# Kernel optimization log

Measured on AMD Instinct MI355X. Metric: run time of the kernel, lower is better.

Reference implementation:

```python
import jax, jax.numpy as jnp
import numpy as np

KSIZE = 3
SCALE = 10.0
EPS = 1e-4


def _prelu(x, a):
    return jnp.where(x >= 0, x, a * x)


def _conv1x1(x, w, b):
    # x: [B,C,H,W], w: [O,C], b: [O]
    return jnp.einsum('bchw,oc->bohw', x, w) + b[None, :, None, None]


def _extract_patches(x, k):
    # same-padded kxk patches, torch-unfold channel-major ordering.
    # x: [B,C,H,W] -> [B, H*W, C, k, k]
    B, C, H, W = x.shape
    p = k // 2
    xp = jnp.pad(x, ((0, 0), (0, 0), (p, p), (p, p)))
    pats = jnp.stack([xp[:, :, i:i + H, j:j + W]
                      for i in range(k) for j in range(k)], axis=2)  # [B,C,k*k,H,W]
    pats = pats.reshape(B, C, k, k, H * W)
    return jnp.transpose(pats, (0, 4, 1, 2, 3))


def setup_inputs() -> dict:
    key = jax.random.key(0)
    ks = jax.random.split(key, 10)
    B, C, r = 4, 64, 2
    H = W = 96
    h = w = 48
    Cr = C // r
    s = 0.05
    return {
        'input': jax.random.normal(ks[0], (B, C, H, W), jnp.float32),
        'small': jax.random.normal(ks[1], (B, C, h, w), jnp.float32),
        'w_match1': jax.random.normal(ks[2], (Cr, C), jnp.float32) * s,
        'b_match1': jax.random.normal(ks[3], (Cr,), jnp.float32) * s,
        'a_match1': jnp.full((1,), 0.25, jnp.float32),
        'w_match2': jax.random.normal(ks[4], (Cr, C), jnp.float32) * s,
        'b_match2': jax.random.normal(ks[5], (Cr,), jnp.float32) * s,
        'a_match2': jnp.full((1,), 0.25, jnp.float32),
        'w_asm': jax.random.normal(ks[6], (C, C), jnp.float32) * s,
        'b_asm': jax.random.normal(ks[7], (C,), jnp.float32) * s,
        'a_asm': jnp.full((1,), 0.25, jnp.float32),
    }


def reference(input, small, w_match1, b_match1, a_match1,
              w_match2, b_match2, a_match2, w_asm, b_asm, a_asm):
    dn = ('NCHW', 'OIHW', 'NCHW')
    pad1 = [(1, 1), (1, 1)]

    match_input = _prelu(_conv1x1(input, w_match1, b_match1), a_match1)  # [B,Cr,H,W]
    embed_w = _prelu(_conv1x1(small, w_asm, b_asm), a_asm)               # [B,C,h,w]
    ref = _prelu(_conv1x1(small, w_match2, b_match2), a_match2)          # [B,Cr,h,w]

    raw_w = _extract_patches(embed_w, KSIZE)  # [B, L, C, 3, 3]  (reconstruction filters)
    w_pat = _extract_patches(ref, KSIZE)      # [B, L, Cr, 3, 3] (matching filters)

    def per_sample(xi, wi, raw_wi):
        # xi: [Cr,H,W], wi: [L,Cr,3,3], raw_wi: [L,C,3,3]
        norm = jnp.sqrt(jnp.sum(wi * wi, axis=(1, 2, 3), keepdims=True))
        wi_n = wi / jnp.maximum(norm, EPS)
        # dynamic conv: correlation of xi with all L normalized patches
        yi = jax.lax.conv_general_dilated(xi[None], wi_n, (1, 1), pad1,
                                          dimension_numbers=dn)  # [1,L,H,W]
        yi = jax.nn.softmax(yi * SCALE, axis=1)
        # conv_transpose2d(yi, raw_wi, stride=2, padding=1):
        # lhs_dilation=2, pad k-1-p=1, spatially flipped, in/out swapped kernel
        wt = jnp.transpose(raw_wi, (1, 0, 2, 3))[:, :, ::-1, ::-1]  # [C,L,3,3]
        out = jax.lax.conv_general_dilated(yi, wt, (1, 1), pad1,
                                           lhs_dilation=(2, 2),
                                           dimension_numbers=dn)  # [1,C,2H-1,2W-1]
        return out[0] / 6.0

    return jax.vmap(per_sample)(match_input, w_pat, raw_w)
```

## Files before the change

kernel.cpp:

```cpp
#include <hip/hip_runtime.h>


typedef unsigned short u16;
typedef __attribute__((ext_vector_type(8))) short short8;
typedef __attribute__((ext_vector_type(8))) _Float16 half8;
typedef __attribute__((ext_vector_type(4))) float f32x4;

__device__ __forceinline__ u16 f2bf(float f) {
    unsigned u = __float_as_uint(f);
    unsigned r = (u + 0x7FFFu + ((u >> 16) & 1u)) >> 16;
    return (u16)r;
}
__device__ __forceinline__ float bf2f(u16 h) {
    return __uint_as_float(((unsigned)h) << 16);
}
__device__ __forceinline__ u16 f2h(float f) {
    _Float16 h = (_Float16)f;
    u16 u; __builtin_memcpy(&u, &h, 2); return u;
}
__device__ __forceinline__ float h2f(u16 u) {
    _Float16 h; __builtin_memcpy(&h, &u, 2); return (float)h;
}

__global__ void kzero(float4* p, long n) {
    long i = (long)blockIdx.x * blockDim.x + threadIdx.x;
    long st = (long)gridDim.x * blockDim.x;
    float4 z; z.x = 0.f; z.y = 0.f; z.z = 0.f; z.w = 0.f;
    for (; i < n; i += st) p[i] = z;
}

__global__ void kmatch(const float* __restrict__ input, const float* __restrict__ w1,
                       const float* __restrict__ b1, const float* __restrict__ a1,
                       u16* __restrict__ xf16) {
    __shared__ float xl[64 * 96];
    __shared__ float wl[32 * 65];
    int b = blockIdx.x / 96, y = blockIdx.x % 96;
    int tid = threadIdx.x;
    for (int i = tid; i < 64 * 96; i += 256) {
        int ci = i / 96, xx = i % 96;
        xl[i] = input[(((b * 64 + ci) * 96) + y) * 96 + xx];
    }
    for (int i = tid; i < 2048; i += 256) wl[(i >> 6) * 65 + (i & 63)] = w1[i];
    __syncthreads();
    float aa = a1[0];
    for (int o = tid; o < 96 * 32; o += 256) {
        int xx = o >> 5, c = o & 31;
        float acc = b1[c];
        #pragma unroll
        for (int ci = 0; ci < 64; ci++) acc = fmaf(xl[ci * 96 + xx], wl[c * 65 + ci], acc);
        float v = acc >= 0.f ? acc : aa * acc;
        xf16[((b * 98 + y + 1) * 98 + (xx + 1)) * 32 + c] = f2h(v);
    }
}

__global__ void ksmall(const float* __restrict__ small, const float* __restrict__ wasm,
                       const float* __restrict__ basm, const float* __restrict__ aasm,
                       const float* __restrict__ wm2, const float* __restrict__ bm2,
                       const float* __restrict__ am2,
                       float* __restrict__ ef32, u16* __restrict__ rkl) {
    __shared__ float sl[64 * 48];
    __shared__ float wa[64 * 65];
    __shared__ float wm[32 * 65];
    int b = blockIdx.x / 48, y = blockIdx.x % 48;
    int tid = threadIdx.x;
    for (int i = tid; i < 64 * 48; i += 256) {
        int ci = i / 48, xx = i % 48;
        sl[i] = small[(((b * 64 + ci) * 48) + y) * 48 + xx];
    }
    for (int i = tid; i < 4096; i += 256) wa[(i >> 6) * 65 + (i & 63)] = wasm[i];
    for (int i = tid; i < 2048; i += 256) wm[(i >> 6) * 65 + (i & 63)] = wm2[i];
    __syncthreads();
    float ae = aasm[0], ar = am2[0];
    for (int o = tid; o < 48 * 64; o += 256) {
        int xx = o >> 6, c = o & 63;
        float acc = basm[c];
        #pragma unroll
        for (int ci = 0; ci < 64; ci++) acc = fmaf(sl[ci * 48 + xx], wa[c * 65 + ci], acc);
        float v = acc >= 0.f ? acc : ae * acc;
        ef32[((b * 50 + y + 1) * 50 + (xx + 1)) * 64 + c] = v;
    }
    for (int o = tid; o < 48 * 32; o += 256) {
        int xx = o >> 5, c = o & 31;
        float acc = bm2[c];
        #pragma unroll
        for (int ci = 0; ci < 64; ci++) acc = fmaf(sl[ci * 48 + xx], wm[c * 65 + ci], acc);
        float v = acc >= 0.f ? acc : ar * acc;
        rkl[((b * 50 + y + 1) * 50 + (xx + 1)) * 32 + c] = f2h(v);
    }
}

__global__ void kinvnorm(const u16* __restrict__ rkl, float* __restrict__ invn) {
    int idx = blockIdx.x * 256 + threadIdx.x;
    int b = idx / 2304, l = idx % 2304;
    int ly = l / 48, lx = l % 48;
    float s = 0.f;
    for (int ty = 0; ty < 3; ty++)
        for (int tx = 0; tx < 3; tx++) {
            int base = ((b * 50 + ly + ty) * 50 + (lx + tx)) * 32;
            #pragma unroll
            for (int c = 0; c < 32; c++) {
                float v = h2f(rkl[base + c]);
                s = fmaf(v, v, s);
            }
        }
    invn[idx] = 10.f / fmaxf(sqrtf(s), 1e-4f);
}

__global__ void kvtp(const float* __restrict__ ef32, u16* __restrict__ vtp) {
    __shared__ float el[3][50 * 64];
    int bi = blockIdx.x;
    int b = bi / 48, ly = bi % 48;
    const float* eb = ef32 + (size_t)b * 50 * 50 * 64;
    int tid = threadIdx.x;
    #pragma unroll
    for (int r = 0; r < 3; ++r)
        for (int i = tid; i < 800; i += 256)
            ((float4*)el[r])[i] = ((const float4*)(eb + (size_t)(ly + r) * 3200))[i];
    __syncthreads();
    u16* vo = vtp + (size_t)b * 576 * 2304 + (size_t)ly * 48;
    for (int n = tid; n < 576; n += 256) {
        int t = n >> 6, c = n & 63;
        int ty = t / 3, tx = t - ty * 3;
        u16* dst = vo + (size_t)n * 2304;
        const float* src = &el[ty][tx * 64 + c];
        #pragma unroll
        for (int g = 0; g < 12; ++g) {
            unsigned lo = (unsigned)f2bf(src[(g * 4 + 0) * 64]) |
                          ((unsigned)f2bf(src[(g * 4 + 1) * 64]) << 16);
            unsigned hi = (unsigned)f2bf(src[(g * 4 + 2) * 64]) |
                          ((unsigned)f2bf(src[(g * 4 + 3) * 64]) << 16);
            uint2 pk; pk.x = lo; pk.y = hi;
            *(uint2*)&dst[g * 4] = pk;
        }
    }
}

__device__ __forceinline__ void stage_ks4(const u16* __restrict__ src, u16* dst, int tid) {
    int wb = tid & ~63;
    #pragma unroll
    for (int k = 0; k < 3; ++k)
        __builtin_amdgcn_global_load_lds(
            (const __attribute__((address_space(1))) void*)(src + (size_t)(tid + k * 256) * 8),
            (__attribute__((address_space(3))) void*)(dst + (size_t)(wb + k * 256) * 8),
            16, 0, 0);
    if (tid < 32)
        __builtin_amdgcn_global_load_lds(
            (const __attribute__((address_space(1))) void*)(src + (size_t)(tid + 768) * 8),
            (__attribute__((address_space(3))) void*)(dst + (size_t)768 * 8),
            16, 0, 0);
}
__device__ __forceinline__ void stage_ks2(const u16* __restrict__ src, u16* dst, int tid) {
    int wb = tid & ~63;
    __builtin_amdgcn_global_load_lds(
        (const __attribute__((address_space(1))) void*)(src + (size_t)tid * 8),
        (__attribute__((address_space(3))) void*)(dst + (size_t)wb * 8),
        16, 0, 0);
    if (tid < 144)
        __builtin_amdgcn_global_load_lds(
            (const __attribute__((address_space(1))) void*)(src + (size_t)(tid + 256) * 8),
            (__attribute__((address_space(3))) void*)(dst + (size_t)(wb + 256) * 8),
            16, 0, 0);
}

__launch_bounds__(256, 2)
__global__ void kfused3(const u16* __restrict__ xf16, const u16* __restrict__ rkl,
                        const u16* __restrict__ vtp, const float* __restrict__ invn,
                        float* __restrict__ Z, int b0, int nb) {
    __shared__ u16 Ks[6][1600];
    __shared__ u16 Pl[2][4608];
    __shared__ u16 Qs[5 * 18 * 32];
    __shared__ float llds[4][16];

    int tid = threadIdx.x;
    int w = tid >> 6, lane = tid & 63, l15 = lane & 15, quad = lane >> 4;
    int bi = blockIdx.x, brel, t;
    if (nb == 4) { brel = bi & 3; t = bi >> 2; }
    else         { brel = 0; t = bi; }
    int b = b0 + brel;
    int px0 = (t % 6) * 16, pyb = (t / 6) * 3;

    const u16* xb = xf16 + (size_t)b * 98 * 98 * 32;
    const u16* rb = rkl + (size_t)b * 50 * 50 * 32;
    const float* invb = invn + b * 2304;
    const u16* vw = vtp + (size_t)b * 576 * 2304 + (size_t)(w * 144 + l15) * 2304 + quad * 8;

    stage_ks4(rb, &Ks[0][0], tid);
    __builtin_amdgcn_sched_barrier(0);

    for (int u = tid; u < 360; u += 256) {
        int cell = u >> 2, ch = u & 3;
        int r = cell / 18, p = cell % 18;
        *(short8*)&Qs[(r * 18 + p) * 32 + ch * 8] =
            *(const short8*)(xb + (((pyb + r) * 98) + (px0 + p)) * 32 + ch * 8);
    }

    int tile = (w < 3) ? w : 2;
    int kh_begin = (w == 3) ? 1 : 0;
    int kh_end   = (w == 2) ? 1 : 2;

    f32x4 acc[27];
    #pragma unroll
    for (int i = 0; i < 27; i++) acc[i] = (f32x4)0.f;
    float lacc[4] = {0.f, 0.f, 0.f, 0.f};

    __syncthreads();

    short8 vv[9];
    int s0 = 0;

    for (int it = 0; it < 24; ++it) {
        int ly0 = it * 2;
        int cur = it & 1;

        float pinv[2][3];
        #pragma unroll
        for (int kh = 0; kh < 2; ++kh)
            #pragma unroll
            for (int lxo = 0; lxo < 3; ++lxo)
                pinv[kh][lxo] = invb[(ly0 + kh) * 48 + lxo * 16 + l15];

        if (it < 23) {
            int s4 = s0 + 4; if (s4 >= 6) s4 -= 6;
            stage_ks2(rb + (size_t)(ly0 + 4) * 1600, &Ks[0][0] + s4 * 1600, tid);
        }
        __builtin_amdgcn_sched_barrier(0x38F);

        const u16* vit = vw + it * 96;
        #pragma unroll
        for (int nt = 0; nt < 9; ++nt) vv[nt] = *(const short8*)(vit + (size_t)nt * 36864);

        u16* Pc = Pl[cur];
        #pragma unroll
        for (int kh = 0; kh < 2; ++kh) {
            if (kh < kh_begin || kh >= kh_end) continue;
            f32x4 sf[3];
            #pragma unroll
            for (int i = 0; i < 3; i++) sf[i] = (f32x4)0.f;
            __builtin_amdgcn_s_setprio(1);
            #pragma unroll
            for (int ty = 0; ty < 3; ++ty) {
                int rr = s0 + kh + ty; if (rr >= 6) rr -= 6;
                const u16* Kr = &Ks[0][0] + rr * 1600;
                #pragma unroll
                for (int tx = 0; tx < 3; ++tx) {
                    half8 a = *(const half8*)&Qs[((tile + ty) * 18 + (l15 + tx)) * 32 + quad * 8];
                    #pragma unroll
                    for (int lxo = 0; lxo < 3; ++lxo) {
                        half8 bb = *(const half8*)&Kr[(lxo * 16 + l15 + tx) * 32 + quad * 8];
                        sf[lxo] = __builtin_amdgcn_mfma_f32_16x16x32_f16(a, bb, sf[lxo], 0, 0, 0);
                    }
                }
            }
            __builtin_amdgcn_s_setprio(0);
            #pragma unroll
            for (int lxo = 0; lxo < 3; ++lxo) {
                float invs = pinv[kh][lxo];
                int k = kh * 48 + lxo * 16 + l15;
                int kb = k >> 5;
                int kc = (k & 31) ^ (quad << 3);
                #pragma unroll
                for (int r = 0; r < 4; ++r) {
                    float p = __expf(sf[lxo][r] * invs);
                    u16 h = f2bf(p);
                    Pc[(tile * 3 + kb) * 512 + (quad * 4 + r) * 32 + kc] = h;
                    lacc[r] += bf2f(h);
                }
            }
        }

        asm volatile("s_waitcnt vmcnt(9) lgkmcnt(0)" ::: "memory");
        __builtin_amdgcn_s_barrier();
        __builtin_amdgcn_sched_barrier(0);

        const u16* Pr = Pl[cur];
        int pcol = l15 * 32 + ((quad ^ (l15 >> 2)) & 3) * 8;
        __builtin_amdgcn_s_setprio(1);
        #pragma unroll
        for (int ks = 0; ks < 3; ++ks) {
            short8 pa0 = *(const short8*)&Pr[(0 * 3 + ks) * 512 + pcol];
            short8 pa1 = *(const short8*)&Pr[(1 * 3 + ks) * 512 + pcol];
            short8 pa2 = *(const short8*)&Pr[(2 * 3 + ks) * 512 + pcol];
            #pragma unroll
            for (int nt = 0; nt < 9; ++nt) {
                short8 vn = vv[nt];
                acc[0 * 9 + nt] = __builtin_amdgcn_mfma_f32_16x16x32_bf16(pa0, vn, acc[0 * 9 + nt], 0, 0, 0);
                acc[1 * 9 + nt] = __builtin_amdgcn_mfma_f32_16x16x32_bf16(pa1, vn, acc[1 * 9 + nt], 0, 0, 0);
                acc[2 * 9 + nt] = __builtin_amdgcn_mfma_f32_16x16x32_bf16(pa2, vn, acc[2 * 9 + nt], 0, 0, 0);
                if (ks < 2)
                    vv[nt] = *(const short8*)(vit + (size_t)nt * 36864 + (ks + 1) * 32);
            }
        }
        __builtin_amdgcn_s_setprio(0);

        s0 += 2; if (s0 >= 6) s0 -= 6;
    }

    #pragma unroll
    for (int r = 0; r < 4; ++r) {
        float v = lacc[r];
        v += __shfl_xor(v, 1);
        v += __shfl_xor(v, 2);
        v += __shfl_xor(v, 4);
        v += __shfl_xor(v, 8);
        lacc[r] = v;
    }
    if (l15 == 0) {
        #pragma unroll
        for (int r = 0; r < 4; ++r)
            llds[w][quad * 4 + r] = lacc[r];
    }
    __syncthreads();
    float* Zb = Z + (size_t)brel * 9216 * 576;
    #pragma unroll
    for (int mt = 0; mt < 3; ++mt) {
        #pragma unroll
        for (int r = 0; r < 4; ++r) {
            int q = (pyb + mt) * 96 + px0 + quad * 4 + r;
            float lsum = (mt < 2) ? llds[mt][quad * 4 + r]
                                  : (llds[2][quad * 4 + r] + llds[3][quad * 4 + r]);
            float rl = 1.0f / (lsum * 6.0f);
            float* zr = Zb + (size_t)q * 576 + w * 144;
            #pragma unroll
            for (int nt = 0; nt < 9; ++nt)
                __builtin_nontemporal_store(acc[mt * 9 + nt][r] * rl, zr + nt * 16 + l15);
        }
    }
}

__global__ void kgather(const float* __restrict__ Z, float* __restrict__ out, int b0) {
    __shared__ float zb[2 * 9 * 580];
    int bi = blockIdx.x;
    int brel = bi / (96 * 12);
    int rem = bi % (96 * 12);
    int b = b0 + brel;
    int q = rem / 12, xt = rem % 12;
    int ox0 = xt * 16, p0 = ox0 >> 1;
    const float* Zb = Z + (size_t)brel * 9216 * 576;
    int tid = threadIdx.x;
    for (int id = tid; id < 2592; id += 256) {
        int pi = id / 1296, r2 = id % 1296;
        int pxi = r2 / 144, n4 = r2 % 144;
        int py = q + pi; if (py > 95) py = 95;
        int px = p0 + pxi; if (px > 95) px = 95;
        *(float4*)&zb[(pi * 9 + pxi) * 580 + n4 * 4] =
            *(const float4*)&Zb[(size_t)(py * 96 + px) * 576 + n4 * 4];
    }
    __syncthreads();
    int xi = tid & 15, cq = tid >> 4;
    int ox = ox0 + xi;
    bool oxv = ox <= 190;
    int ntx, txl[2], pxl[2];
    if (xi & 1) { ntx = 2; txl[0] = 0; pxl[0] = (xi + 1) >> 1; txl[1] = 2; pxl[1] = (xi - 1) >> 1; }
    else        { ntx = 1; txl[0] = 1; pxl[0] = xi >> 1; txl[1] = 1; pxl[1] = xi >> 1; }
    int oy0 = 2 * q;
    #pragma unroll
    for (int ck = 0; ck < 4; ++ck) {
        int c = cq + ck * 16;
        float v0 = 0.f, v1 = 0.f;
        for (int j = 0; j < ntx; ++j) {
            int tx = txl[j], pxi = pxl[j];
            v0 += zb[(0 * 9 + pxi) * 580 + (3 + tx) * 64 + c];
            v1 += zb[(1 * 9 + pxi) * 580 + (0 + tx) * 64 + c];
            v1 += zb[(0 * 9 + pxi) * 580 + (6 + tx) * 64 + c];
        }
        if (oxv) {
            float* o = out + (((size_t)(b * 64 + c) * 191 + oy0) * 191 + ox);
            *o = v0;
            if (q < 95) *(o + 191) = v1;
        }
    }
}

extern "C" void kernel_launch(void* const* d_in, const int* in_sizes, int n_in,
                              void* d_out, int out_size, void* d_ws, size_t ws_size,
                              hipStream_t stream) {
    const float* input = (const float*)d_in[0];
    const float* small = (const float*)d_in[1];
    const float* w1 = (const float*)d_in[2];
    const float* b1 = (const float*)d_in[3];
    const float* a1 = (const float*)d_in[4];
    const float* w2 = (const float*)d_in[5];
    const float* b2 = (const float*)d_in[6];
    const float* a2 = (const float*)d_in[7];
    const float* wa = (const float*)d_in[8];
    const float* ba = (const float*)d_in[9];
    const float* aa = (const float*)d_in[10];

    char* ws = (char*)d_ws;
    u16* xf16 = (u16*)(ws + 0);
    u16* rkl = (u16*)(ws + 2458624);
    float* ef = (float*)(ws + 3098624);
    u16* vtp = (u16*)(ws + 5658624);
    float* invn = (float*)(ws + 16275456);
    const size_t PREP = 16312320;
    float* Zbuf = (float*)(ws + PREP);
    float* out = (float*)d_out;

    int nb = (ws_size >= (size_t)101246976) ? 4 : 1;

    kzero<<<1024, 256, 0, stream>>>((float4*)ws, 5658624 / 16);
    kmatch<<<384, 256, 0, stream>>>(input, w1, b1, a1, xf16);
    ksmall<<<192, 256, 0, stream>>>(small, wa, ba, aa, w2, b2, a2, ef, rkl);
    kinvnorm<<<36, 256, 0, stream>>>(rkl, invn);
    kvtp<<<192, 256, 0, stream>>>(ef, vtp);

    for (int b0 = 0; b0 < 4; b0 += nb) {
        kfused3<<<nb * 192, 256, 0, stream>>>(xf16, rkl, vtp, invn, Zbuf, b0, nb);
        kgather<<<nb * 1152, 256, 0, stream>>>(Zbuf, out, b0);
    }
}
```

Baseline: 471.1 us.

## Process four key rows per iteration with one key row per wave

The main loop now handles four key rows per iteration, 12 iterations instead of 24. Each wave owns one key row and computes scores for all three query tiles, so the uneven tile/kh split across waves is gone. The K ring buffer grows to 10 rows and the P buffer doubles so each PV step covers a 192-wide K chunk. Softmax partial sums are now kept per tile and summed across all four waves. Per-iteration barriers are halved, at the cost of much more LDS per block, which could limit occupancy, and more register pressure.

```diff
diff --git a/kernel.cpp b/kernel.cpp
--- a/kernel.cpp
+++ b/kernel.cpp
@@ -166,10 +166,10 @@
 __global__ void kfused3(const u16* __restrict__ xf16, const u16* __restrict__ rkl,
                         const u16* __restrict__ vtp, const float* __restrict__ invn,
                         float* __restrict__ Z, int b0, int nb) {
-    __shared__ u16 Ks[6][1600];
-    __shared__ u16 Pl[2][4608];
+    __shared__ u16 Ks[10][1600];
+    __shared__ u16 Pl[2][9216];
     __shared__ u16 Qs[5 * 18 * 32];
-    __shared__ float llds[4][16];
+    __shared__ float llds[4][3][16];
 
     int tid = threadIdx.x;
     int w = tid >> 6, lane = tid & 63, l15 = lane & 15, quad = lane >> 4;
@@ -185,6 +185,7 @@
     const u16* vw = vtp + (size_t)b * 576 * 2304 + (size_t)(w * 144 + l15) * 2304 + quad * 8;
 
     stage_ks4(rb, &Ks[0][0], tid);
+    stage_ks2(rb + (size_t)4 * 1600, &Ks[4][0], tid);
     __builtin_amdgcn_sched_barrier(0);
 
     for (int u = tid; u < 360; u += 256) {
@@ -194,52 +195,51 @@
             *(const short8*)(xb + (((pyb + r) * 98) + (px0 + p)) * 32 + ch * 8);
     }
 
-    int tile = (w < 3) ? w : 2;
-    int kh_begin = (w == 3) ? 1 : 0;
-    int kh_end   = (w == 2) ? 1 : 2;
-
     f32x4 acc[27];
     #pragma unroll
     for (int i = 0; i < 27; i++) acc[i] = (f32x4)0.f;
-    float lacc[4] = {0.f, 0.f, 0.f, 0.f};
+    float lacc[3][4];
+    #pragma unroll
+    for (int i = 0; i < 3; i++)
+        #pragma unroll
+        for (int r = 0; r < 4; r++) lacc[i][r] = 0.f;
 
     __syncthreads();
 
     short8 vv[9];
     int s0 = 0;
 
-    for (int it = 0; it < 24; ++it) {
-        int ly0 = it * 2;
+    for (int it = 0; it < 12; ++it) {
+        int ly0 = it * 4;
         int cur = it & 1;
 
-        float pinv[2][3];
-        #pragma unroll
-        for (int kh = 0; kh < 2; ++kh)
-            #pragma unroll
-            for (int lxo = 0; lxo < 3; ++lxo)
-                pinv[kh][lxo] = invb[(ly0 + kh) * 48 + lxo * 16 + l15];
-
-        if (it < 23) {
-            int s4 = s0 + 4; if (s4 >= 6) s4 -= 6;
-            stage_ks2(rb + (size_t)(ly0 + 4) * 1600, &Ks[0][0] + s4 * 1600, tid);
+        float pinv[3];
+        #pragma unroll
+        for (int lxo = 0; lxo < 3; ++lxo)
+            pinv[lxo] = invb[(ly0 + w) * 48 + lxo * 16 + l15];
+
+        if (it < 11) {
+            int s6 = s0 + 6; if (s6 >= 10) s6 -= 10;
+            int s8 = s0 + 8; if (s8 >= 10) s8 -= 10;
+            stage_ks2(rb + (size_t)(ly0 + 6) * 1600, &Ks[0][0] + s6 * 1600, tid);
+            stage_ks2(rb + (size_t)(ly0 + 8) * 1600, &Ks[0][0] + s8 * 1600, tid);
         }
         __builtin_amdgcn_sched_barrier(0x38F);
 
-        const u16* vit = vw + it * 96;
+        const u16* vit = vw + it * 192;
         #pragma unroll
         for (int nt = 0; nt < 9; ++nt) vv[nt] = *(const short8*)(vit + (size_t)nt * 36864);
 
         u16* Pc = Pl[cur];
         #pragma unroll
-        for (int kh = 0; kh < 2; ++kh) {
-            if (kh < kh_begin || kh >= kh_end) continue;
+        for (int tile = 0; tile < 3; ++tile) {
             f32x4 sf[3];
             #pragma unroll
             for (int i = 0; i < 3; i++) sf[i] = (f32x4)0.f;
             __builtin_amdgcn_s_setprio(1);
             #pragma unroll
             for (int ty = 0; ty < 3; ++ty) {
-                int rr = s0 + kh + ty; if (rr >= 6) rr -= 6;
+                int rr = s0 + w + ty; if (rr >= 10) rr -= 10;
                 const u16* Kr = &Ks[0][0] + rr * 1600;
                 #pragma unroll
                 for (int tx = 0; tx < 3; ++tx) {
@@ -254,16 +254,16 @@
             __builtin_amdgcn_s_setprio(0);
             #pragma unroll
             for (int lxo = 0; lxo < 3; ++lxo) {
-                float invs = pinv[kh][lxo];
-                int k = kh * 48 + lxo * 16 + l15;
+                float invs = pinv[lxo];
+                int k = w * 48 + lxo * 16 + l15;
                 int kb = k >> 5;
                 int kc = (k & 31) ^ (quad << 3);
                 #pragma unroll
                 for (int r = 0; r < 4; ++r) {
                     float p = __expf(sf[lxo][r] * invs);
                     u16 h = f2bf(p);
-                    Pc[(tile * 3 + kb) * 512 + (quad * 4 + r) * 32 + kc] = h;
-                    lacc[r] += bf2f(h);
+                    Pc[(tile * 6 + kb) * 512 + (quad * 4 + r) * 32 + kc] = h;
+                    lacc[tile][r] += bf2f(h);
                 }
             }
         }
@@ -276,38 +276,42 @@
         int pcol = l15 * 32 + ((quad ^ (l15 >> 2)) & 3) * 8;
         __builtin_amdgcn_s_setprio(1);
         #pragma unroll
-        for (int ks = 0; ks < 3; ++ks) {
-            short8 pa0 = *(const short8*)&Pr[(0 * 3 + ks) * 512 + pcol];
-            short8 pa1 = *(const short8*)&Pr[(1 * 3 + ks) * 512 + pcol];
-            short8 pa2 = *(const short8*)&Pr[(2 * 3 + ks) * 512 + pcol];
+        for (int ks = 0; ks < 6; ++ks) {
+            short8 pa0 = *(const short8*)&Pr[(0 * 6 + ks) * 512 + pcol];
+            short8 pa1 = *(const short8*)&Pr[(1 * 6 + ks) * 512 + pcol];
+            short8 pa2 = *(const short8*)&Pr[(2 * 6 + ks) * 512 + pcol];
             #pragma unroll
             for (int nt = 0; nt < 9; ++nt) {
                 short8 vn = vv[nt];
                 acc[0 * 9 + nt] = __builtin_amdgcn_mfma_f32_16x16x32_bf16(pa0, vn, acc[0 * 9 + nt], 0, 0, 0);
                 acc[1 * 9 + nt] = __builtin_amdgcn_mfma_f32_16x16x32_bf16(pa1, vn, acc[1 * 9 + nt], 0, 0, 0);
                 acc[2 * 9 + nt] = __builtin_amdgcn_mfma_f32_16x16x32_bf16(pa2, vn, acc[2 * 9 + nt], 0, 0, 0);
-                if (ks < 2)
+                if (ks < 5)
                     vv[nt] = *(const short8*)(vit + (size_t)nt * 36864 + (ks + 1) * 32);
             }
         }
         __builtin_amdgcn_s_setprio(0);
 
-        s0 += 2; if (s0 >= 6) s0 -= 6;
-    }
-
-    #pragma unroll
-    for (int r = 0; r < 4; ++r) {
-        float v = lacc[r];
-        v += __shfl_xor(v, 1);
-        v += __shfl_xor(v, 2);
-        v += __shfl_xor(v, 4);
-        v += __shfl_xor(v, 8);
-        lacc[r] = v;
-    }
+        s0 += 4; if (s0 >= 10) s0 -= 10;
+    }
+
+    #pragma unroll
+    for (int tile = 0; tile < 3; ++tile)
+        #pragma unroll
+        for (int r = 0; r < 4; ++r) {
+            float v = lacc[tile][r];
+            v += __shfl_xor(v, 1);
+            v += __shfl_xor(v, 2);
+            v += __shfl_xor(v, 4);
+            v += __shfl_xor(v, 8);
+            lacc[tile][r] = v;
+        }
     if (l15 == 0) {
         #pragma unroll
-        for (int r = 0; r < 4; ++r)
-            llds[w][quad * 4 + r] = lacc[r];
+        for (int tile = 0; tile < 3; ++tile)
+            #pragma unroll
+            for (int r = 0; r < 4; ++r)
+                llds[w][tile][quad * 4 + r] = lacc[tile][r];
     }
     __syncthreads();
     float* Zb = Z + (size_t)brel * 9216 * 576;
@@ -316,8 +320,8 @@
         #pragma unroll
         for (int r = 0; r < 4; ++r) {
             int q = (pyb + mt) * 96 + px0 + quad * 4 + r;
-            float lsum = (mt < 2) ? llds[mt][quad * 4 + r]
-                                  : (llds[2][quad * 4 + r] + llds[3][quad * 4 + r]);
+            int m = quad * 4 + r;
+            float lsum = llds[0][mt][m] + llds[1][mt][m] + llds[2][mt][m] + llds[3][mt][m];
             float rl = 1.0f / (lsum * 6.0f);
             float* zr = Zb + (size_t)q * 576 + w * 144;
             #pragma unroll
```

Result: no change. 463.6 us (-1.6%).
